# Kernel optimization log

Measured on AMD Instinct MI355X. Metric: run time of the kernel, lower is better.

The kernel has to match this reference:

```python
import jax, jax.numpy as jnp
import numpy as np

N = 50000
D = 128
E = 600000
ALPHA = 0.1
THETA = 0.5
LAYER = 1


def setup_inputs() -> dict:
    key = jax.random.key(0)
    k1, k2, k3, k4, k5, k6 = jax.random.split(key, 6)
    x = jax.random.normal(k1, (N, D), dtype=jnp.float32)
    x0 = jax.random.normal(k2, (N, D), dtype=jnp.float32)
    edge_index = jax.random.randint(k3, (2, E), 0, N, dtype=jnp.int64)
    norm = jax.random.uniform(k4, (E,), dtype=jnp.float32)
    # Linear weight, torch nn.Linear default init: U(-1/sqrt(fan_in), 1/sqrt(fan_in))
    bound = 1.0 / np.sqrt(D)
    W = jax.random.uniform(k5, (D, D), dtype=jnp.float32, minval=-bound, maxval=bound)
    return {"x": x, "x0": x0, "edge_index": edge_index, "norm": norm, "W": W}


def reference(x, x0, edge_index, norm, W):
    row, col = edge_index[0], edge_index[1]
    # gather source features, scale per-edge, scatter-add into destinations
    msgs = x[row] * norm[:, None]                      # [E, D]
    h = jax.ops.segment_sum(msgs, col, num_segments=N)  # [N, D]
    h = (1.0 - ALPHA) * h + ALPHA * x0
    beta = np.log(THETA / LAYER + 1.0).astype(np.float32)
    # lin(h) = h @ W.T (torch Linear applies x @ W^T)
    h = (1.0 - beta) * h + beta * (h @ W.T)
    return h
```

## Files before the change

### kernel.cpp

```cpp
#include <hip/hip_runtime.h>

#define DIM 128
#define ALPHA 0.1f
#define BETA 0.40546510810816438f

typedef __attribute__((ext_vector_type(8))) short short8v;
typedef __attribute__((ext_vector_type(4))) float float4v;

static __device__ inline unsigned short f2bf(float f) {
  union { float f; unsigned u; } a;
  a.f = f;
  unsigned r = a.u + 0x7fff + ((a.u >> 16) & 1);
  return (unsigned short)(r >> 16);
}

__global__ __launch_bounds__(256) void prep(const int* __restrict__ col,
                                            int* __restrict__ counts,
                                            const float* __restrict__ x,
                                            short* __restrict__ xb,
                                            const float* __restrict__ W,
                                            short* __restrict__ Wb,
                                            int E, int total4, int cntBlocks,
                                            int cvtXBlocks) {
  int b = blockIdx.x;
  if (b < cntBlocks) {
    int e = b * 256 + threadIdx.x;
    if (e < E) atomicAdd(&counts[col[e]], 1);
  } else if (b < cntBlocks + cvtXBlocks) {
    int i = (b - cntBlocks) * 256 + threadIdx.x;
    if (i < total4) {
      float4 v = ((const float4*)x)[i];
      ((short4*)xb)[i] = make_short4((short)f2bf(v.x), (short)f2bf(v.y),
                                     (short)f2bf(v.z), (short)f2bf(v.w));
    }
  } else {
    int i = (b - cntBlocks - cvtXBlocks) * 256 + threadIdx.x;
    if (i < 128 * 32) {
      float4 v = ((const float4*)W)[i];
      ((short4*)Wb)[i] = make_short4((short)f2bf(v.x), (short)f2bf(v.y),
                                     (short)f2bf(v.z), (short)f2bf(v.w));
    }
  }
}

__global__ __launch_bounds__(256) void scan_blocks(const int* __restrict__ counts,
                                                   int* __restrict__ offsets,
                                                   int* __restrict__ blockSums, int N) {
  __shared__ int sm[256];
  int tid = threadIdx.x;
  int gid = blockIdx.x * 256 + tid;
  int v = (gid < N) ? counts[gid] : 0;
  sm[tid] = v;
  __syncthreads();
  for (int off = 1; off < 256; off <<= 1) {
    int t = (tid >= off) ? sm[tid - off] : 0;
    __syncthreads();
    sm[tid] += t;
    __syncthreads();
  }
  if (gid < N) offsets[gid] = sm[tid] - v;
  if (tid == 255) blockSums[blockIdx.x] = sm[255];
}

__global__ __launch_bounds__(256) void scan_off(int* __restrict__ offsets,
                                                const int* __restrict__ blockSums,
                                                int* __restrict__ cursor,
                                                int N, int E, int nb) {
  __shared__ int sm[256];
  int tid = threadIdx.x;
  int v = (tid < nb) ? blockSums[tid] : 0;
  sm[tid] = v;
  __syncthreads();
  for (int off = 1; off < 256; off <<= 1) {
    int t = (tid >= off) ? sm[tid - off] : 0;
    __syncthreads();
    sm[tid] += t;
    __syncthreads();
  }
  int excl = sm[tid] - v;
  __syncthreads();
  sm[tid] = excl;
  __syncthreads();
  int pref = sm[blockIdx.x];

  int gid = blockIdx.x * 256 + tid;
  if (gid < N) {
    offsets[gid] += pref;
    cursor[gid] = 0;
  } else if (gid == N) {
    offsets[N] = E;
  }
}

__global__ __launch_bounds__(256) void fill_edges(const int* __restrict__ row,
                                                  const int* __restrict__ col,
                                                  const float* __restrict__ nrm,
                                                  const int* __restrict__ offsets,
                                                  int* __restrict__ cursor,
                                                  int2* __restrict__ emeta, int E) {
  int e = blockIdx.x * 256 + threadIdx.x;
  if (e >= E) return;
  int c = col[e];
  int p = atomicAdd(&cursor[c], 1);
  int idx = offsets[c] + p;
  float s = (1.0f - ALPHA) * nrm[e];
  emeta[idx] = make_int2(row[e], __float_as_int(s));
}

__global__ __launch_bounds__(256) void gather_gemm(const unsigned* __restrict__ xb,
                                                   const float* __restrict__ x0,
                                                   const int* __restrict__ offs,
                                                   const int2* __restrict__ emeta,
                                                   const short* __restrict__ Wb,
                                                   float* __restrict__ out, int N) {
  __shared__ unsigned short hb[16][136];
  const int tid = threadIdx.x;
  const int lane = tid & 63;
  const int wave = tid >> 6;
  const int row0 = blockIdx.x * 16;

  for (int q = 0; q < 4; ++q) {
    const int lr = wave * 4 + q;
    const int n = row0 + lr;
    unsigned packed = 0;
    if (n < N) {
      int s = offs[n], t = offs[n + 1];
      float accx[8], accy[8];
#pragma unroll
      for (int j = 0; j < 8; ++j) { accx[j] = 0.0f; accy[j] = 0.0f; }
      for (int base = s; base < t; base += 64) {
        int r = 0;
        float sc = 0.0f;
        if (base + lane < t) {
          int2 m = emeta[base + lane];
          r = m.x;
          sc = __int_as_float(m.y);
        }
        int cnt = t - base;
        if (cnt > 64) cnt = 64;
        int cnt8 = (cnt + 7) & ~7;
        for (int i = 0; i < cnt8; i += 8) {
#pragma unroll
          for (int j = 0; j < 8; ++j) {
            int rj = __shfl(r, i + j);
            float sj = __shfl(sc, i + j);
            unsigned u = xb[(size_t)rj * (DIM / 2) + lane];
            accx[j] += sj * __uint_as_float(u << 16);
            accy[j] += sj * __uint_as_float(u & 0xffff0000u);
          }
        }
      }
      float sx = ((accx[0] + accx[1]) + (accx[2] + accx[3])) +
                 ((accx[4] + accx[5]) + (accx[6] + accx[7]));
      float sy = ((accy[0] + accy[1]) + (accy[2] + accy[3])) +
                 ((accy[4] + accy[5]) + (accy[6] + accy[7]));
      float2 v0 = *(const float2*)(x0 + (size_t)n * DIM + 2 * lane);
      float hx = sx + ALPHA * v0.x;
      float hy = sy + ALPHA * v0.y;
      packed = (unsigned)f2bf(hx) | ((unsigned)f2bf(hy) << 16);
    }
    *(unsigned*)&hb[lr][2 * lane] = packed;
  }
  __syncthreads();

  const int arow = lane & 15;
  const int kg = (lane >> 4) * 8;
  short8v a[4];
#pragma unroll
  for (int s = 0; s < 4; ++s) a[s] = *(const short8v*)&hb[arow][s * 32 + kg];

#pragma unroll
  for (int j2 = 0; j2 < 2; ++j2) {
    const int jt = wave * 2 + j2;
    const int bcol = jt * 16 + (lane & 15);
    float4v acc = {0.0f, 0.0f, 0.0f, 0.0f};
#pragma unroll
    for (int s = 0; s < 4; ++s) {
      short8v b = *(const short8v*)(Wb + (size_t)bcol * DIM + s * 32 + kg);
      acc = __builtin_amdgcn_mfma_f32_16x16x32_bf16(a[s], b, acc, 0, 0, 0);
    }
    const int lr0 = (lane >> 4) << 2;
#pragma unroll
    for (int p = 0; p < 4; ++p) {
      int R = row0 + lr0 + p;
      if (R < N) {
        int c = jt * 16 + (lane & 15);
        float hv = __uint_as_float(((unsigned)hb[lr0 + p][c]) << 16);
        out[(size_t)R * DIM + c] = (1.0f - BETA) * hv + BETA * acc[p];
      }
    }
  }
}

__global__ __launch_bounds__(256) void count_edges(const int* __restrict__ col,
                                                   int* __restrict__ counts, int E) {
  int e = blockIdx.x * 256 + threadIdx.x;
  if (e < E) atomicAdd(&counts[col[e]], 1);
}

__global__ __launch_bounds__(256) void gather_nodes_f32(const float* __restrict__ x,
                                                        const float* __restrict__ x0,
                                                        const int* __restrict__ offs,
                                                        const int2* __restrict__ emeta,
                                                        float* __restrict__ h, int N) {
  int lane = threadIdx.x & 63;
  int gwave = blockIdx.x * 4 + (threadIdx.x >> 6);
  int nwaves = gridDim.x * 4;
  int dbase = 2 * lane;
  for (int n = gwave; n < N; n += nwaves) {
    int s = offs[n], t = offs[n + 1];
    float ax = 0, ay = 0, bx = 0, by = 0, cx = 0, cy = 0, dx = 0, dy = 0;
    for (int base = s; base < t; base += 64) {
      int r = 0;
      float sc = 0.0f;
      if (base + lane < t) {
        int2 m = emeta[base + lane];
        r = m.x;
        sc = __int_as_float(m.y);
      }
      int cnt = t - base;
      if (cnt > 64) cnt = 64;
      int cnt4 = (cnt + 3) & ~3;
      for (int i = 0; i < cnt4; i += 4) {
        int r0 = __shfl(r, i), r1 = __shfl(r, i + 1);
        int r2 = __shfl(r, i + 2), r3 = __shfl(r, i + 3);
        float s0 = __shfl(sc, i), s1 = __shfl(sc, i + 1);
        float s2 = __shfl(sc, i + 2), s3 = __shfl(sc, i + 3);
        float2 v0 = *(const float2*)(x + (size_t)r0 * DIM + dbase);
        float2 v1 = *(const float2*)(x + (size_t)r1 * DIM + dbase);
        float2 v2 = *(const float2*)(x + (size_t)r2 * DIM + dbase);
        float2 v3 = *(const float2*)(x + (size_t)r3 * DIM + dbase);
        ax += s0 * v0.x; ay += s0 * v0.y;
        bx += s1 * v1.x; by += s1 * v1.y;
        cx += s2 * v2.x; cy += s2 * v2.y;
        dx += s3 * v3.x; dy += s3 * v3.y;
      }
    }
    float2 v0 = *(const float2*)(x0 + (size_t)n * DIM + dbase);
    float2 hv;
    hv.x = ((ax + bx) + (cx + dx)) + ALPHA * v0.x;
    hv.y = ((ay + by) + (cy + dy)) + ALPHA * v0.y;
    *(float2*)(h + (size_t)n * DIM + dbase) = hv;
  }
}

__global__ __launch_bounds__(256) void final_mfma(const float* __restrict__ W,
                                                  float* __restrict__ out, int N) {
  __shared__ short W_s[128][136];
  __shared__ short h_s[64][136];
  const int tid = threadIdx.x;
  const int lane = tid & 63;
  const int wave = tid >> 6;
  const int row0 = blockIdx.x * 64;

  for (int idx = tid; idx < 128 * 32; idx += 256) {
    int r = idx >> 5, c4 = idx & 31;
    float4 v = ((const float4*)(W + (size_t)r * DIM))[c4];
    *(short4*)&W_s[r][c4 * 4] = make_short4((short)f2bf(v.x), (short)f2bf(v.y),
                                            (short)f2bf(v.z), (short)f2bf(v.w));
  }
  for (int idx = tid; idx < 64 * 32; idx += 256) {
    int r = idx >> 5, c4 = idx & 31;
    int R = row0 + r;
    short4 sv = make_short4(0, 0, 0, 0);
    if (R < N) {
      float4 v = ((const float4*)(out + (size_t)R * DIM))[c4];
      sv = make_short4((short)f2bf(v.x), (short)f2bf(v.y), (short)f2bf(v.z),
                       (short)f2bf(v.w));
    }
    *(short4*)&h_s[r][c4 * 4] = sv;
  }
  __syncthreads();

  const int wr0 = wave * 16;
  const int arow = wr0 + (lane & 15);
  const int kg = (lane >> 4) * 8;
  short8v a[4];
#pragma unroll
  for (int s = 0; s < 4; ++s) a[s] = *(const short8v*)&h_s[arow][s * 32 + kg];

#pragma unroll
  for (int jt = 0; jt < 8; ++jt) {
    const int bcol = jt * 16 + (lane & 15);
    float4v acc = {0.0f, 0.0f, 0.0f, 0.0f};
#pragma unroll
    for (int s = 0; s < 4; ++s) {
      short8v b = *(const short8v*)&W_s[bcol][s * 32 + kg];
      acc = __builtin_amdgcn_mfma_f32_16x16x32_bf16(a[s], b, acc, 0, 0, 0);
    }
    const int rbase = row0 + wr0 + ((lane >> 4) << 2);
#pragma unroll
    for (int p = 0; p < 4; ++p) {
      int R = rbase + p;
      if (R < N) {
        size_t off = (size_t)R * DIM + jt * 16 + (lane & 15);
        out[off] = (1.0f - BETA) * out[off] + BETA * acc[p];
      }
    }
  }
}

__global__ __launch_bounds__(256) void init_h(const float* __restrict__ x0,
                                              float* __restrict__ h, int total4) {
  int i = blockIdx.x * 256 + threadIdx.x;
  if (i < total4) {
    float4 v = ((const float4*)x0)[i];
    v.x *= ALPHA; v.y *= ALPHA; v.z *= ALPHA; v.w *= ALPHA;
    ((float4*)h)[i] = v;
  }
}

__global__ __launch_bounds__(256) void scatter_edges(const float* __restrict__ x,
                                                     const int* __restrict__ row,
                                                     const int* __restrict__ col,
                                                     const float* __restrict__ nrm,
                                                     float* __restrict__ h, int E) {
  int gid = blockIdx.x * 256 + threadIdx.x;
  int e = gid >> 5;
  if (e >= E) return;
  int d4 = (gid & 31) << 2;
  int r = row[e];
  int c = col[e];
  float s = (1.0f - ALPHA) * nrm[e];
  const float4 v = *(const float4*)(x + (size_t)r * DIM + d4);
  float* dst = h + (size_t)c * DIM + d4;
  atomicAdd(dst + 0, s * v.x);
  atomicAdd(dst + 1, s * v.y);
  atomicAdd(dst + 2, s * v.z);
  atomicAdd(dst + 3, s * v.w);
}

extern "C" void kernel_launch(void* const* d_in, const int* in_sizes, int n_in,
                              void* d_out, int out_size, void* d_ws, size_t ws_size,
                              hipStream_t stream) {
  const float* x = (const float*)d_in[0];
  const float* x0 = (const float*)d_in[1];
  const int* ei = (const int*)d_in[2];
  const float* nrm = (const float*)d_in[3];
  const float* W = (const float*)d_in[4];
  float* out = (float*)d_out;

  const int N = in_sizes[0] / DIM;
  const int E = in_sizes[2] / 2;
  const int* row = ei;
  const int* col = ei + E;

  const size_t csrNeed =
      (size_t)(2 * (N + 1) + 256 + N) * sizeof(int) + (size_t)E * 8;
  const size_t fullNeed =
      csrNeed + (size_t)N * DIM * sizeof(short) + 128 * 128 * sizeof(short);

  const int eBlocks = (E + 255) / 256;
  const int nBlocks = (N + 255) / 256;
  const int n1Blocks = (N + 256) / 256;

  if (ws_size >= csrNeed && nBlocks <= 256) {
    int* counts = (int*)d_ws;
    int* offsets = counts + (N + 1);
    int* blockSums = offsets + (N + 1);
    int* cursor = blockSums + 256;
    int2* emeta = (int2*)(cursor + N);
    short* xb = (short*)(emeta + E);
    short* Wb = xb + (size_t)N * DIM;

    hipMemsetAsync(counts, 0, (size_t)(N + 1) * sizeof(int), stream);

    if (ws_size >= fullNeed) {
      const int total4 = N * DIM / 4;
      const int cvtXBlocks = (total4 + 255) / 256;
      const int prepBlocks = eBlocks + cvtXBlocks + 16;
      hipLaunchKernelGGL(prep, dim3(prepBlocks), dim3(256), 0, stream, col, counts, x, xb, W, Wb,
                         E, total4, eBlocks, cvtXBlocks);
      hipLaunchKernelGGL(scan_blocks, dim3(nBlocks), dim3(256), 0, stream, counts, offsets,
                         blockSums, N);
      hipLaunchKernelGGL(scan_off, dim3(n1Blocks), dim3(256), 0, stream, offsets, blockSums,
                         cursor, N, E, nBlocks);
      hipLaunchKernelGGL(fill_edges, dim3(eBlocks), dim3(256), 0, stream, row, col, nrm, offsets,
                         cursor, emeta, E);
      const int t16 = (N + 15) / 16;
      hipLaunchKernelGGL(gather_gemm, dim3(t16), dim3(256), 0, stream, (const unsigned*)xb, x0,
                         offsets, emeta, Wb, out, N);
    } else {
      hipLaunchKernelGGL(count_edges, dim3(eBlocks), dim3(256), 0, stream, col, counts, E);
      hipLaunchKernelGGL(scan_blocks, dim3(nBlocks), dim3(256), 0, stream, counts, offsets,
                         blockSums, N);
      hipLaunchKernelGGL(scan_off, dim3(n1Blocks), dim3(256), 0, stream, offsets, blockSums,
                         cursor, N, E, nBlocks);
      hipLaunchKernelGGL(fill_edges, dim3(eBlocks), dim3(256), 0, stream, row, col, nrm, offsets,
                         cursor, emeta, E);
      const int gBlocks = (N + 3) / 4;
      hipLaunchKernelGGL(gather_nodes_f32, dim3(gBlocks), dim3(256), 0, stream, x, x0, offsets,
                         emeta, out, N);
      hipLaunchKernelGGL(final_mfma, dim3((N + 63) / 64), dim3(256), 0, stream, W, out, N);
    }
  } else {
    int total4 = N * DIM / 4;
    hipLaunchKernelGGL(init_h, dim3((total4 + 255) / 256), dim3(256), 0, stream, x0, out, total4);
    long long threads = (long long)E * 32;
    hipLaunchKernelGGL(scatter_edges, dim3((int)((threads + 255) / 256)), dim3(256), 0, stream, x,
                       row, col, nrm, out, E);
    hipLaunchKernelGGL(final_mfma, dim3((N + 63) / 64), dim3(256), 0, stream, W, out, N);
  }
}
```

Before: 125.7 us.

## Record per-edge rank during counting and read edge metadata directly in gather

The counting atomic now stores its return value as a per-edge rank, so fill_edges places each edge at offsets[c]+rank[e] without a second atomic pass over a cursor array. The cursor reset in scan_off is removed. The gather loops stop loading 64 edges cooperatively and broadcasting them with shuffles; each wave now loads emeta entries directly as uniform loads, with an unrolled main loop and a scalar tail, and the x0 load is moved earlier. This adds an E-sized rank buffer to the workspace and relies on the uniform emeta loads being cheap.

```diff
diff --git a/kernel.cpp b/kernel.cpp
--- a/kernel.cpp
+++ b/kernel.cpp
@@ -16,6 +16,7 @@
 
 __global__ __launch_bounds__(256) void prep(const int* __restrict__ col,
                                             int* __restrict__ counts,
+                                            int* __restrict__ rank,
                                             const float* __restrict__ x,
                                             short* __restrict__ xb,
                                             const float* __restrict__ W,
@@ -25,7 +26,7 @@
   int b = blockIdx.x;
   if (b < cntBlocks) {
     int e = b * 256 + threadIdx.x;
-    if (e < E) atomicAdd(&counts[col[e]], 1);
+    if (e < E) rank[e] = atomicAdd(&counts[col[e]], 1);
   } else if (b < cntBlocks + cvtXBlocks) {
     int i = (b - cntBlocks) * 256 + threadIdx.x;
     if (i < total4) {
@@ -64,7 +65,6 @@
 
 __global__ __launch_bounds__(256) void scan_off(int* __restrict__ offsets,
                                                 const int* __restrict__ blockSums,
-                                                int* __restrict__ cursor,
                                                 int N, int E, int nb) {
   __shared__ int sm[256];
   int tid = threadIdx.x;
@@ -84,25 +84,20 @@
   int pref = sm[blockIdx.x];
 
   int gid = blockIdx.x * 256 + tid;
-  if (gid < N) {
-    offsets[gid] += pref;
-    cursor[gid] = 0;
-  } else if (gid == N) {
-    offsets[N] = E;
-  }
+  if (gid < N) offsets[gid] += pref;
+  else if (gid == N) offsets[N] = E;
 }
 
 __global__ __launch_bounds__(256) void fill_edges(const int* __restrict__ row,
                                                   const int* __restrict__ col,
                                                   const float* __restrict__ nrm,
                                                   const int* __restrict__ offsets,
-                                                  int* __restrict__ cursor,
+                                                  const int* __restrict__ rank,
                                                   int2* __restrict__ emeta, int E) {
   int e = blockIdx.x * 256 + threadIdx.x;
   if (e >= E) return;
   int c = col[e];
-  int p = atomicAdd(&cursor[c], 1);
-  int idx = offsets[c] + p;
+  int idx = offsets[c] + rank[e];
   float s = (1.0f - ALPHA) * nrm[e];
   emeta[idx] = make_int2(row[e], __float_as_int(s));
 }
@@ -124,37 +119,33 @@
     const int n = row0 + lr;
     unsigned packed = 0;
     if (n < N) {
-      int s = offs[n], t = offs[n + 1];
+      const int s = offs[n], t = offs[n + 1];
+      float2 v0 = *(const float2*)(x0 + (size_t)n * DIM + 2 * lane);
       float accx[8], accy[8];
 #pragma unroll
       for (int j = 0; j < 8; ++j) { accx[j] = 0.0f; accy[j] = 0.0f; }
-      for (int base = s; base < t; base += 64) {
-        int r = 0;
-        float sc = 0.0f;
-        if (base + lane < t) {
-          int2 m = emeta[base + lane];
-          r = m.x;
-          sc = __int_as_float(m.y);
+      int i = s;
+      for (; i + 8 <= t; i += 8) {
+#pragma unroll
+        for (int j = 0; j < 8; ++j) {
+          int2 m = emeta[i + j];
+          float sj = __int_as_float(m.y);
+          unsigned u = xb[(size_t)m.x * (DIM / 2) + lane];
+          accx[j] += sj * __uint_as_float(u << 16);
+          accy[j] += sj * __uint_as_float(u & 0xffff0000u);
         }
-        int cnt = t - base;
-        if (cnt > 64) cnt = 64;
-        int cnt8 = (cnt + 7) & ~7;
-        for (int i = 0; i < cnt8; i += 8) {
-#pragma unroll
-          for (int j = 0; j < 8; ++j) {
-            int rj = __shfl(r, i + j);
-            float sj = __shfl(sc, i + j);
-            unsigned u = xb[(size_t)rj * (DIM / 2) + lane];
-            accx[j] += sj * __uint_as_float(u << 16);
-            accy[j] += sj * __uint_as_float(u & 0xffff0000u);
-          }
-        }
+      }
+      for (; i < t; ++i) {
+        int2 m = emeta[i];
+        float sj = __int_as_float(m.y);
+        unsigned u = xb[(size_t)m.x * (DIM / 2) + lane];
+        accx[0] += sj * __uint_as_float(u << 16);
+        accy[0] += sj * __uint_as_float(u & 0xffff0000u);
       }
       float sx = ((accx[0] + accx[1]) + (accx[2] + accx[3])) +
                  ((accx[4] + accx[5]) + (accx[6] + accx[7]));
       float sy = ((accy[0] + accy[1]) + (accy[2] + accy[3])) +
                  ((accy[4] + accy[5]) + (accy[6] + accy[7]));
-      float2 v0 = *(const float2*)(x0 + (size_t)n * DIM + 2 * lane);
       float hx = sx + ALPHA * v0.x;
       float hy = sy + ALPHA * v0.y;
       packed = (unsigned)f2bf(hx) | ((unsigned)f2bf(hy) << 16);
@@ -193,9 +184,10 @@
 }
 
 __global__ __launch_bounds__(256) void count_edges(const int* __restrict__ col,
-                                                   int* __restrict__ counts, int E) {
+                                                   int* __restrict__ counts,
+                                                   int* __restrict__ rank, int E) {
   int e = blockIdx.x * 256 + threadIdx.x;
-  if (e < E) atomicAdd(&counts[col[e]], 1);
+  if (e < E) rank[e] = atomicAdd(&counts[col[e]], 1);
 }
 
 __global__ __launch_bounds__(256) void gather_nodes_f32(const float* __restrict__ x,
@@ -209,37 +201,28 @@
   int dbase = 2 * lane;
   for (int n = gwave; n < N; n += nwaves) {
     int s = offs[n], t = offs[n + 1];
-    float ax = 0, ay = 0, bx = 0, by = 0, cx = 0, cy = 0, dx = 0, dy = 0;
-    for (int base = s; base < t; base += 64) {
-      int r = 0;
-      float sc = 0.0f;
-      if (base + lane < t) {
-        int2 m = emeta[base + lane];
-        r = m.x;
-        sc = __int_as_float(m.y);
-      }
-      int cnt = t - base;
-      if (cnt > 64) cnt = 64;
-      int cnt4 = (cnt + 3) & ~3;
-      for (int i = 0; i < cnt4; i += 4) {
-        int r0 = __shfl(r, i), r1 = __shfl(r, i + 1);
-        int r2 = __shfl(r, i + 2), r3 = __shfl(r, i + 3);
-        float s0 = __shfl(sc, i), s1 = __shfl(sc, i + 1);
-        float s2 = __shfl(sc, i + 2), s3 = __shfl(sc, i + 3);
-        float2 v0 = *(const float2*)(x + (size_t)r0 * DIM + dbase);
-        float2 v1 = *(const float2*)(x + (size_t)r1 * DIM + dbase);
-        float2 v2 = *(const float2*)(x + (size_t)r2 * DIM + dbase);
-        float2 v3 = *(const float2*)(x + (size_t)r3 * DIM + dbase);
-        ax += s0 * v0.x; ay += s0 * v0.y;
-        bx += s1 * v1.x; by += s1 * v1.y;
-        cx += s2 * v2.x; cy += s2 * v2.y;
-        dx += s3 * v3.x; dy += s3 * v3.y;
-      }
+    float ax = 0, ay = 0, bx = 0, by = 0;
+    int i = s;
+    for (; i + 4 <= t; i += 4) {
+      int2 m0 = emeta[i], m1 = emeta[i + 1], m2 = emeta[i + 2], m3 = emeta[i + 3];
+      float2 v0 = *(const float2*)(x + (size_t)m0.x * DIM + dbase);
+      float2 v1 = *(const float2*)(x + (size_t)m1.x * DIM + dbase);
+      float2 v2 = *(const float2*)(x + (size_t)m2.x * DIM + dbase);
+      float2 v3 = *(const float2*)(x + (size_t)m3.x * DIM + dbase);
+      ax += __int_as_float(m0.y) * v0.x; ay += __int_as_float(m0.y) * v0.y;
+      bx += __int_as_float(m1.y) * v1.x; by += __int_as_float(m1.y) * v1.y;
+      ax += __int_as_float(m2.y) * v2.x; ay += __int_as_float(m2.y) * v2.y;
+      bx += __int_as_float(m3.y) * v3.x; by += __int_as_float(m3.y) * v3.y;
+    }
+    for (; i < t; ++i) {
+      int2 m = emeta[i];
+      float2 v = *(const float2*)(x + (size_t)m.x * DIM + dbase);
+      ax += __int_as_float(m.y) * v.x; ay += __int_as_float(m.y) * v.y;
     }
     float2 v0 = *(const float2*)(x0 + (size_t)n * DIM + dbase);
     float2 hv;
-    hv.x = ((ax + bx) + (cx + dx)) + ALPHA * v0.x;
-    hv.y = ((ay + by) + (cy + dy)) + ALPHA * v0.y;
+    hv.x = (ax + bx) + ALPHA * v0.x;
+    hv.y = (ay + by) + ALPHA * v0.y;
     *(float2*)(h + (size_t)n * DIM + dbase) = hv;
   }
 }
@@ -346,7 +329,7 @@
   const int* col = ei + E;
 
   const size_t csrNeed =
-      (size_t)(2 * (N + 1) + 256 + N) * sizeof(int) + (size_t)E * 8;
+      (size_t)(2 * (N + 1) + 256 + E) * sizeof(int) + (size_t)E * 8;
   const size_t fullNeed =
       csrNeed + (size_t)N * DIM * sizeof(short) + 128 * 128 * sizeof(short);
 
@@ -358,8 +341,8 @@
     int* counts = (int*)d_ws;
     int* offsets = counts + (N + 1);
     int* blockSums = offsets + (N + 1);
-    int* cursor = blockSums + 256;
-    int2* emeta = (int2*)(cursor + N);
+    int* rank = blockSums + 256;
+    int2* emeta = (int2*)(rank + E);
     short* xb = (short*)(emeta + E);
     short* Wb = xb + (size_t)N * DIM;
 
@@ -369,25 +352,25 @@
       const int total4 = N * DIM / 4;
       const int cvtXBlocks = (total4 + 255) / 256;
       const int prepBlocks = eBlocks + cvtXBlocks + 16;
-      hipLaunchKernelGGL(prep, dim3(prepBlocks), dim3(256), 0, stream, col, counts, x, xb, W, Wb,
-                         E, total4, eBlocks, cvtXBlocks);
+      hipLaunchKernelGGL(prep, dim3(prepBlocks), dim3(256), 0, stream, col, counts, rank, x, xb,
+                         W, Wb, E, total4, eBlocks, cvtXBlocks);
       hipLaunchKernelGGL(scan_blocks, dim3(nBlocks), dim3(256), 0, stream, counts, offsets,
                          blockSums, N);
-      hipLaunchKernelGGL(scan_off, dim3(n1Blocks), dim3(256), 0, stream, offsets, blockSums,
-                         cursor, N, E, nBlocks);
+      hipLaunchKernelGGL(scan_off, dim3(n1Blocks), dim3(256), 0, stream, offsets, blockSums, N, E,
+                         nBlocks);
       hipLaunchKernelGGL(fill_edges, dim3(eBlocks), dim3(256), 0, stream, row, col, nrm, offsets,
-                         cursor, emeta, E);
+                         rank, emeta, E);
       const int t16 = (N + 15) / 16;
       hipLaunchKernelGGL(gather_gemm, dim3(t16), dim3(256), 0, stream, (const unsigned*)xb, x0,
                          offsets, emeta, Wb, out, N);
     } else {
-      hipLaunchKernelGGL(count_edges, dim3(eBlocks), dim3(256), 0, stream, col, counts, E);
+      hipLaunchKernelGGL(count_edges, dim3(eBlocks), dim3(256), 0, stream, col, counts, rank, E);
       hipLaunchKernelGGL(scan_blocks, dim3(nBlocks), dim3(256), 0, stream, counts, offsets,
                          blockSums, N);
-      hipLaunchKernelGGL(scan_off, dim3(n1Blocks), dim3(256), 0, stream, offsets, blockSums,
-                         cursor, N, E, nBlocks);
+      hipLaunchKernelGGL(scan_off, dim3(n1Blocks), dim3(256), 0, stream, offsets, blockSums, N, E,
+                         nBlocks);
       hipLaunchKernelGGL(fill_edges, dim3(eBlocks), dim3(256), 0, stream, row, col, nrm, offsets,
-                         cursor, emeta, E);
+                         rank, emeta, E);
       const int gBlocks = (N + 3) / 4;
       hipLaunchKernelGGL(gather_nodes_f32, dim3(gBlocks), dim3(256), 0, stream, x, x0, offsets,
                          emeta, out, N);
```

Result: faster. 119.4 us (-5.0%).
